# Kernel optimization log

Measured on AMD Instinct MI355X. Metric: run time of the kernel, lower is better.

The kernel has to match this reference:

```python
import jax, jax.numpy as jnp
import numpy as np

T, B, L, CTX, H = 512, 512, 16, 64, 128
STATE_DIM, SHOT, PID, DATA = 32, 12, 35, 23


def setup_inputs() -> dict:
    key = jax.random.key(0)
    ks = jax.random.split(key, 64)
    k = iter(ks)
    def rn(shape, s=0.1):
        return (jax.random.normal(next(k), shape) * s).astype(jnp.float32)
    xs = jax.random.normal(next(k), (T, B, DATA), jnp.float32)
    xs = xs.at[:, :, 12].set(jax.random.randint(next(k), (T, B), 0, SHOT).astype(jnp.float32))
    xs = xs.at[:, :, 17].set(jax.random.randint(next(k), (T, B), 0, PID).astype(jnp.float32))
    xs = xs.at[:, :, 20].set(jax.random.randint(next(k), (T, B), 0, SHOT).astype(jnp.float32))
    return dict(
        total_xs=jnp.zeros((1,), jnp.float32),
        xs=xs,
        ts=jnp.linspace(0.0, 2.0, T).astype(jnp.float32),
        noise_std=jnp.asarray(0.1, jnp.float32),
        z0_noise=jax.random.normal(next(k), (B, L), jnp.float32),
        bm_noise=jax.random.normal(next(k), (T - 1, B, L), jnp.float32),
        shot_emb=rn((SHOT, 8)), player_emb=rn((PID, 8)),
        gru_wih=rn((3 * H, STATE_DIM)), gru_whh=rn((3 * H, H)),
        gru_bih=rn((3 * H,)), gru_bhh=rn((3 * H,)),
        enc_w=rn((CTX, H)), enc_b=rn((CTX,)),
        qz0_w=rn((2 * L, CTX)), qz0_b=rn((2 * L,)),
        f_w1=rn((H, L + CTX)), f_b1=rn((H,)), f_w2=rn((H, H)), f_b2=rn((H,)),
        f_w3=rn((L, H)), f_b3=rn((L,)),
        h_w1=rn((H, L)), h_b1=rn((H,)), h_w2=rn((H, H)), h_b2=rn((H,)),
        h_w3=rn((L, H)), h_b3=rn((L,)),
        g_w1=rn((L, H)), g_b1=rn((L, H)), g_w2=rn((L, H)), g_b2=rn((L,)),
        proj_w=rn((STATE_DIM, L)), proj_b=rn((STATE_DIM,)),
        pz0_mean=jnp.zeros((1, L), jnp.float32), pz0_logstd=jnp.zeros((1, L), jnp.float32),
        act_w=rn((128, L)), act_b=rn((128,)),
        act_land_w=rn((2, 128)), act_shot_w=rn((SHOT, 128)), act_move_w=rn((2, 128)),
    )


def _forward(xs, noise_std, shot_emb, player_emb, gru_wih, gru_whh, gru_bih, gru_bhh,
             enc_w, enc_b, qz0_w, qz0_b,
             f_w1, f_b1, f_w2, f_b2, f_w3, f_b3,
             h_w1, h_b1, h_w2, h_b2, h_w3, h_b3,
             g_w1, g_b1, g_w2, g_b2,
             proj_w, proj_b, pz0_mean, pz0_logstd,
             act_w, act_b, act_land_w, act_shot_w, act_move_w,
             ts, z0_noise, bm_noise):
    # --- SDE_embed_and_transform: replace shot/player id cols with embeddings ---
    state = xs[:, :, :18]
    shot_ids = state[:, :, 12].astype(jnp.int32)
    pid_ids = state[:, :, 17].astype(jnp.int32)
    state_t = jnp.concatenate([state[:, :, :12], shot_emb[shot_ids],
                               state[:, :, 13:17], player_emb[pid_ids]], axis=-1)  # (T,B,32)
    xs_t = jnp.concatenate([state_t, xs[:, :, 18:]], axis=-1)  # (T,B,37)
    # --- Encoder: GRU over time-reversed states, linear head, flip back ---
    def gru_step(h, xt):
        gi = xt @ gru_wih.T + gru_bih
        gh = h @ gru_whh.T + gru_bhh
        ir, iz, inn = jnp.split(gi, 3, axis=-1)
        hr, hz, hn = jnp.split(gh, 3, axis=-1)
        r = jax.nn.sigmoid(ir + hr)
        zg = jax.nn.sigmoid(iz + hz)
        n = jnp.tanh(inn + r * hn)
        hnew = (1.0 - zg) * n + zg * h
        return hnew, hnew
    h0 = jnp.zeros((xs.shape[1], gru_whh.shape[1]), xs.dtype)
    _, hs = jax.lax.scan(gru_step, h0, state_t[::-1])
    ctx = (hs @ enc_w.T + enc_b)[::-1]  # (T,B,CTX)
    # --- posterior z0 ---
    qm, qls = jnp.split(ctx[0] @ qz0_w.T + qz0_b, 2, axis=1)
    z0 = qm + jnp.exp(qls) * z0_noise
    # --- Euler-Maruyama with logqp; searchsorted(right) -> ctx[min(i+1,T-1)] = ctx[i+1] ---
    dts = ts[1:] - ts[:-1]  # (T-1,)
    dW = jnp.sqrt(dts)[:, None, None] * bm_noise
    ctx_steps = ctx[1:]
    def mlp3(x, w1, b1, w2, b2, w3, b3):
        h1 = jax.nn.softplus(x @ w1.T + b1)
        h2 = jax.nn.softplus(h1 @ w2.T + b2)
        return h2 @ w3.T + b3
    def g_diag(y):  # (B,L): per-latent-dim scalar nets, batched over L
        hg = jax.nn.softplus(y[:, :, None] * g_w1[None] + g_b1[None])  # (B,L,H)
        return jax.nn.sigmoid(jnp.einsum('blh,lh->bl', hg, g_w2) + g_b2)
    def sde_step(z, inp):
        c, dw, dt = inp
        f_val = mlp3(jnp.concatenate([z, c], axis=1), f_w1, f_b1, f_w2, f_b2, f_w3, f_b3)
        h_val = mlp3(z, h_w1, h_b1, h_w2, h_b2, h_w3, h_b3)
        g_val = g_diag(z)
        u = (f_val - h_val) / g_val
        logr = 0.5 * jnp.sum(u * u, axis=1) * dt
        z_new = z + f_val * dt + g_val * dw
        return z_new, (z_new, logr)
    _, (z_tail, log_ratio) = jax.lax.scan(sde_step, z0, (ctx_steps, dW, dts))
    zs = jnp.concatenate([z0[None], z_tail], axis=0)  # (T,B,L)
    _xs = zs @ proj_w.T + proj_b  # (T,B,32)
    # --- action model losses ---
    a = jax.nn.relu(zs @ act_w.T + act_b)
    land = (a @ act_land_w.T).reshape(-1, 2)
    shot_logits = (a @ act_shot_w.T).reshape(-1, act_shot_w.shape[0])
    move = (a @ act_move_w.T).reshape(-1, 2)
    true_actions = xs_t[:, :, -5:]
    true_land = true_actions[:, :, :2].reshape(-1, 2)
    true_move = true_actions[:, :, 3:].reshape(-1, 2)
    true_shot = true_actions[:, :, 2].astype(jnp.int32).reshape(-1)
    land_loss = jnp.mean((land - true_land) ** 2)
    move_loss = jnp.mean((move - true_move) ** 2)
    logp = jax.nn.log_softmax(shot_logits, axis=-1)
    picked = jnp.take_along_axis(logp, true_shot[:, None], axis=1)[:, 0]
    mask = (true_shot != 0).astype(logp.dtype)  # CrossEntropy ignore_index=0
    shot_loss = -jnp.sum(picked * mask) / jnp.maximum(jnp.sum(mask), 1.0)
    # --- reconstruction log-likelihood ---
    xs_state = xs_t[:, :, :STATE_DIM]
    LOG2PI = 1.8378770664093453
    log_pxs = jnp.mean(jnp.sum(
        -0.5 * ((xs_state - _xs) / noise_std) ** 2 - jnp.log(noise_std) - 0.5 * LOG2PI,
        axis=(0, 2)))
    # --- KL(q(z0) || p(z0)) ---
    var_q = jnp.exp(2.0 * qls)
    var_p = jnp.exp(2.0 * pz0_logstd)
    kl = pz0_logstd - qls + (var_q + (qm - pz0_mean) ** 2) / (2.0 * var_p) - 0.5
    logqp0 = jnp.mean(jnp.sum(kl, axis=1))
    logqp_path = jnp.mean(jnp.sum(log_ratio, axis=0))
    return log_pxs, logqp0 + logqp_path + land_loss + shot_loss + move_loss


def reference(total_xs, xs, ts, noise_std, z0_noise, bm_noise, shot_emb, player_emb,
              gru_wih, gru_whh, gru_bih, gru_bhh, enc_w, enc_b, qz0_w, qz0_b,
              f_w1, f_b1, f_w2, f_b2, f_w3, f_b3, h_w1, h_b1, h_w2, h_b2, h_w3, h_b3,
              g_w1, g_b1, g_w2, g_b2, proj_w, proj_b, pz0_mean, pz0_logstd,
              act_w, act_b, act_land_w, act_shot_w, act_move_w):
    return _forward(xs, noise_std, shot_emb, player_emb, gru_wih, gru_whh, gru_bih, gru_bhh,
                    enc_w, enc_b, qz0_w, qz0_b,
                    f_w1, f_b1, f_w2, f_b2, f_w3, f_b3,
                    h_w1, h_b1, h_w2, h_b2, h_w3, h_b3,
                    g_w1, g_b1, g_w2, g_b2,
                    proj_w, proj_b, pz0_mean, pz0_logstd,
                    act_w, act_b, act_land_w, act_shot_w, act_move_w,
                    ts, z0_noise, bm_noise)
```

## Files before the change

kernel.cpp:

```cpp
#include <hip/hip_runtime.h>
#include <cstdint>

typedef _Float16 f16;
typedef _Float16 f16x2 __attribute__((ext_vector_type(2)));

#define T_STEPS 512
#define B_SZ 512
#define LOG2PI 1.8378770664093453f

__device__ __forceinline__ uint32_t packh2(float a, float b) {
  f16x2 v; v[0] = (f16)a; v[1] = (f16)b;
  return __builtin_bit_cast(uint32_t, v);
}

__device__ __forceinline__ float fdot2(uint32_t a, uint32_t b, float c) {
#if defined(__AMDGCN__) && __has_builtin(__builtin_amdgcn_fdot2)
  return __builtin_amdgcn_fdot2(__builtin_bit_cast(f16x2, a),
                                __builtin_bit_cast(f16x2, b), c, false);
#else
  f16x2 x = __builtin_bit_cast(f16x2, a), y = __builtin_bit_cast(f16x2, b);
  return c + (float)x[0] * (float)y[0] + (float)x[1] * (float)y[1];
#endif
}

#define DOT4(acc, w0, w1, w2, w3, v)                                     \
  do {                                                                   \
    acc = fdot2((w0), (v).x, acc); acc = fdot2((w1), (v).y, acc);        \
    acc = fdot2((w2), (v).z, acc); acc = fdot2((w3), (v).w, acc);        \
  } while (0)

__device__ __forceinline__ float sigmoidf_(float x) {
  return 1.0f / (1.0f + __expf(-x));
}
__device__ __forceinline__ float tanhf_(float x) {
  float ax = fabsf(x);
  float t = __expf(-2.0f * ax);
  float r = (1.0f - t) / (1.0f + t);
  return copysignf(r, x);
}
__device__ __forceinline__ float softplusf_(float x) {
  return fmaxf(x, 0.0f) + __logf(1.0f + __expf(-fabsf(x)));
}

__global__ __launch_bounds__(256) void k_embed(
    const float* __restrict__ xs, const float* __restrict__ shot_emb,
    const float* __restrict__ player_emb, f16* __restrict__ state_t,
    float* __restrict__ accums) {
  if (blockIdx.x == 0 && threadIdx.x < 16) accums[threadIdx.x] = 0.0f;
  size_t idx = (size_t)blockIdx.x * 256 + threadIdx.x;
  const float* xp = xs + idx * 23;
  f16* op = state_t + idx * 32;
  int sid = (int)xp[12];
  int pid = (int)xp[17];
#pragma unroll
  for (int i = 0; i < 12; ++i) op[i] = (f16)xp[i];
  const float* se = shot_emb + sid * 8;
#pragma unroll
  for (int i = 0; i < 8; ++i) op[12 + i] = (f16)se[i];
#pragma unroll
  for (int i = 0; i < 4; ++i) op[20 + i] = (f16)xp[13 + i];
  const float* pe = player_emb + pid * 8;
#pragma unroll
  for (int i = 0; i < 8; ++i) op[24 + i] = (f16)pe[i];
}

__global__ __launch_bounds__(512) void k_gru(
    const f16* __restrict__ state_t, const float* __restrict__ wih,
    const float* __restrict__ whh, const float* __restrict__ bih,
    const float* __restrict__ bhh, const float* __restrict__ enc_w,
    const float* __restrict__ enc_b, const float* __restrict__ qz0_w,
    const float* __restrict__ qz0_b, const float* __restrict__ z0_noise,
    const float* __restrict__ pz0_mean, const float* __restrict__ pz0_logstd,
    f16* __restrict__ ctx, float* __restrict__ z0_out,
    float* __restrict__ accums) {
  __shared__ uint32_t s_x[2][16];
  __shared__ uint32_t s_h[2][64];
  __shared__ float s_gates[2 * 128 * 4];
  __shared__ float s_encp[2 * 64 * 2];
  __shared__ float s_ctx0[2][64];
  __shared__ float s_q[2][32];

  const int tid = threadIdx.x;
  const int bbase = blockIdx.x * 2;
  const uint32_t* stu = (const uint32_t*)state_t;

  uint32_t wA[64];
  uint32_t wB[16];
  float bias0 = 0.f, bias1 = 0.f, encbr = 0.f;

  if (tid < 256) {
    int g = tid >> 7, du = tid & 127;
    const float* whr = whh + (size_t)(g * 128 + du) * 128;
#pragma unroll
    for (int i = 0; i < 64; ++i) wA[i] = packh2(whr[2 * i], whr[2 * i + 1]);
    const float* wxr = wih + (size_t)(g * 128 + du) * 32;
#pragma unroll
    for (int i = 0; i < 16; ++i) wB[i] = packh2(wxr[2 * i], wxr[2 * i + 1]);
    bias0 = bih[g * 128 + du] + bhh[g * 128 + du];
  } else if (tid < 384) {
    int du = tid - 256;
    const float* whr = whh + (size_t)(256 + du) * 128;
#pragma unroll
    for (int i = 0; i < 64; ++i) wA[i] = packh2(whr[2 * i], whr[2 * i + 1]);
    const float* wxr = wih + (size_t)(256 + du) * 32;
#pragma unroll
    for (int i = 0; i < 16; ++i) wB[i] = packh2(wxr[2 * i], wxr[2 * i + 1]);
    bias0 = bih[256 + du];
    bias1 = bhh[256 + du];
  } else {
    int e = tid - 384, c = e & 63, ks = e >> 6;
    const float* wer = enc_w + (size_t)c * 128 + ks * 64;
#pragma unroll
    for (int i = 0; i < 32; ++i) wA[i] = packh2(wer[2 * i], wer[2 * i + 1]);
    encbr = enc_b[c];
  }

  if (tid < 128) s_h[tid >> 6][tid & 63] = 0u;
  if (tid < 32) {
    int b = tid >> 4, i = tid & 15;
    s_x[b][i] = stu[((size_t)(T_STEPS - 1) * B_SZ + bbase + b) * 16 + i];
  }
  float h_old = 0.0f;
  __syncthreads();

  for (int t = T_STEPS - 1; t >= 0; --t) {
    uint4 xpref = make_uint4(0, 0, 0, 0);
    if (tid < 256) {
      int g = tid >> 7, du = tid & 127;
#pragma unroll
      for (int b = 0; b < 2; ++b) {
        float a = bias0;
        const uint4* xq = (const uint4*)&s_x[b][0];
#pragma unroll
        for (int j = 0; j < 4; ++j) {
          uint4 v = xq[j];
          DOT4(a, wB[4 * j], wB[4 * j + 1], wB[4 * j + 2], wB[4 * j + 3], v);
        }
        const uint4* hq = (const uint4*)&s_h[b][0];
#pragma unroll
        for (int j = 0; j < 16; ++j) {
          uint4 v = hq[j];
          DOT4(a, wA[4 * j], wA[4 * j + 1], wA[4 * j + 2], wA[4 * j + 3], v);
        }
        s_gates[(b * 128 + du) * 4 + g] = a;
      }
    } else if (tid < 384) {
      int du = tid - 256;
#pragma unroll
      for (int b = 0; b < 2; ++b) {
        float aI = bias0, aH = bias1;
        const uint4* xq = (const uint4*)&s_x[b][0];
#pragma unroll
        for (int j = 0; j < 4; ++j) {
          uint4 v = xq[j];
          DOT4(aI, wB[4 * j], wB[4 * j + 1], wB[4 * j + 2], wB[4 * j + 3], v);
        }
        const uint4* hq = (const uint4*)&s_h[b][0];
#pragma unroll
        for (int j = 0; j < 16; ++j) {
          uint4 v = hq[j];
          DOT4(aH, wA[4 * j], wA[4 * j + 1], wA[4 * j + 2], wA[4 * j + 3], v);
        }
        s_gates[(b * 128 + du) * 4 + 2] = aI;
        s_gates[(b * 128 + du) * 4 + 3] = aH;
      }
    } else {
      int e = tid - 384, ks = e >> 6, cc = e & 63;
      (void)cc;
      if (t < T_STEPS - 1) {
#pragma unroll
        for (int b = 0; b < 2; ++b) {
          float a = 0.f;
          const uint4* hq = (const uint4*)&s_h[b][ks * 32];
#pragma unroll
          for (int j = 0; j < 8; ++j) {
            uint4 v = hq[j];
            DOT4(a, wA[4 * j], wA[4 * j + 1], wA[4 * j + 2], wA[4 * j + 3], v);
          }
          s_encp[(b * 64 + cc) * 2 + ks] = a;
        }
      }
      if (e < 8 && t > 0) {
        int b = e & 1, q = e >> 1;
        xpref = *(const uint4*)(stu +
                                ((size_t)(t - 1) * B_SZ + bbase + b) * 16 + q * 4);
      }
    }
    __syncthreads();
    if (tid < 256) {
      int b = tid >> 7, du = tid & 127;
      const float4 gt = *(const float4*)&s_gates[(b * 128 + du) * 4];
      float r = sigmoidf_(gt.x), zg = sigmoidf_(gt.y);
      float n = tanhf_(gt.z + r * gt.w);
      float hnew = (1.0f - zg) * n + zg * h_old;
      h_old = hnew;
      ((f16*)&s_h[b][0])[du] = (f16)hnew;
    } else if (tid >= 384) {
      int e = tid - 384, cc = e & 63, b = e >> 6;
      if (t < T_STEPS - 1) {
        float2 p = *(const float2*)&s_encp[(b * 64 + cc) * 2];
        ctx[((size_t)(t + 1) * B_SZ + bbase + b) * 64 + cc] =
            (f16)(p.x + p.y + encbr);
      }
      if (e < 8 && t > 0) {
        int b2 = e & 1, q = e >> 1;
        *(uint4*)&s_x[b2][q * 4] = xpref;
      }
    }
    __syncthreads();
  }

  if (tid >= 384) {
    int e = tid - 384, ks = e >> 6, cc = e & 63;
#pragma unroll
    for (int b = 0; b < 2; ++b) {
      float a = 0.f;
      const uint4* hq = (const uint4*)&s_h[b][ks * 32];
#pragma unroll
      for (int j = 0; j < 8; ++j) {
        uint4 v = hq[j];
        DOT4(a, wA[4 * j], wA[4 * j + 1], wA[4 * j + 2], wA[4 * j + 3], v);
      }
      s_encp[(b * 64 + cc) * 2 + ks] = a;
    }
  }
  __syncthreads();
  if (tid >= 384) {
    int e = tid - 384, cc = e & 63, b = e >> 6;
    float2 p = *(const float2*)&s_encp[(b * 64 + cc) * 2];
    float val = p.x + p.y + encbr;
    ctx[((size_t)bbase + b) * 64 + cc] = (f16)val;
    s_ctx0[b][cc] = val;
  }
  __syncthreads();
  if (tid < 64) {
    int b = tid >> 5, o = tid & 31;
    float acc = qz0_b[o];
#pragma unroll 8
    for (int k = 0; k < 64; ++k) acc += qz0_w[o * 64 + k] * s_ctx0[b][k];
    s_q[b][o] = acc;
  }
  __syncthreads();
  if (tid < 32) {
    int b = tid >> 4, l = tid & 15;
    int bg = bbase + b;
    float qm = s_q[b][l], qls = s_q[b][16 + l];
    float z0v = qm + __expf(qls) * z0_noise[bg * 16 + l];
    z0_out[bg * 16 + l] = z0v;
    float pm = pz0_mean[l], pls = pz0_logstd[l];
    float var_q = __expf(2.0f * qls);
    float var_p = __expf(2.0f * pls);
    float dm = qm - pm;
    float kl = pls - qls + (var_q + dm * dm) / (2.0f * var_p) - 0.5f;
    atomicAdd(&accums[5], kl);
  }
}

__global__ __launch_bounds__(512) void k_sde(
    const f16* __restrict__ ctx, const float* __restrict__ z0_in,
    const float* __restrict__ ts, const float* __restrict__ bm_noise,
    const float* __restrict__ fw1, const float* __restrict__ fb1,
    const float* __restrict__ fw2, const float* __restrict__ fb2,
    const float* __restrict__ fw3, const float* __restrict__ fb3,
    const float* __restrict__ hw1, const float* __restrict__ hb1,
    const float* __restrict__ hw2, const float* __restrict__ hb2,
    const float* __restrict__ hw3, const float* __restrict__ hb3,
    const float* __restrict__ gw1, const float* __restrict__ gb1,
    const float* __restrict__ gw2, const float* __restrict__ gb2,
    f16* __restrict__ zs, float* __restrict__ accums) {
  __shared__ uint32_t s_x2[2][40];
  __shared__ float s_zf[2][16];
  __shared__ uint32_t s_h1[2][2][64];
  __shared__ uint32_t s_h2[2][2][64];
  __shared__ float s_gp[256];
  __shared__ float s_gv[32];
  __shared__ float s_p2[2 * 2 * 128 * 2];
  __shared__ float s_p3[2 * 2 * 16 * 8];
  __shared__ float s_dts[512];

  const int tid = threadIdx.x;
  const int bbase = blockIdx.x * 2;

  uint32_t uw[48];
  uint32_t wP2[32];
  uint32_t wP3[8];
  float bias1r = 0.f, bias2r = 0.f, gb2r = 0.f, fb3r = 0.f, hb3r = 0.f;

  if (tid < 256) {
    int l = tid & 15, k8 = (tid >> 4) & 7;
#pragma unroll
    for (int i = 0; i < 16; ++i) {
      int h = k8 * 16 + i;
      uw[i] = __builtin_bit_cast(uint32_t, gw1[l * 128 + h]);
      uw[16 + i] = __builtin_bit_cast(uint32_t, gb1[l * 128 + h]);
      uw[32 + i] = __builtin_bit_cast(uint32_t, gw2[l * 128 + h]);
    }
  } else if (tid < 384) {
    int u = tid - 256;
    const float* w = fw1 + (size_t)u * 80;
#pragma unroll
    for (int i = 0; i < 40; ++i) uw[i] = packh2(w[2 * i], w[2 * i + 1]);
    bias1r = fb1[u];
  } else {
    int u = tid - 384;
    const float* w = hw1 + (size_t)u * 16;
#pragma unroll
    for (int i = 0; i < 8; ++i) uw[i] = packh2(w[2 * i], w[2 * i + 1]);
    bias1r = hb1[u];
  }
  {
    int u = tid & 127, ks = (tid >> 7) & 1, mlp = tid >> 8;
    const float* w = (mlp ? hw2 : fw2) + (size_t)u * 128 + ks * 64;
#pragma unroll
    for (int i = 0; i < 32; ++i) wP2[i] = packh2(w[2 * i], w[2 * i + 1]);
    bias2r = (mlp ? hb2 : fb2)[u];
  }
  if (tid < 128 || (tid >= 256 && tid < 384)) {
    int o = tid & 15, k8 = (tid >> 4) & 7;
    const float* w = ((tid >= 256) ? hw3 : fw3) + (size_t)o * 128 + k8 * 16;
#pragma unroll
    for (int i = 0; i < 8; ++i) wP3[i] = packh2(w[2 * i], w[2 * i + 1]);
  }
  if (tid >= 128 && tid < 160) gb2r = gb2[tid & 15];
  if (tid < 32) {
    fb3r = fb3[tid & 15];
    hb3r = hb3[tid & 15];
  }

  if (tid < 511) s_dts[tid] = ts[tid + 1] - ts[tid];
  float bmc = 0.f;
  uint4 cpref = make_uint4(0, 0, 0, 0);
  if (tid < 32) {
    int b = tid >> 4, l = tid & 15, bg = bbase + b;
    float z = z0_in[bg * 16 + l];
    s_zf[b][l] = z;
    ((f16*)&s_x2[b][0])[l] = (f16)z;
    zs[(size_t)bg * 16 + l] = (f16)z;
    bmc = bm_noise[((size_t)0 * B_SZ + bg) * 16 + l];
  }
  if (tid >= 32 && tid < 48) {
    int i = tid - 32, b = i & 1, q = i >> 1;
    const uint32_t* cu = (const uint32_t*)ctx;
    uint4 v = *(const uint4*)(cu + ((size_t)1 * B_SZ + bbase + b) * 32 + q * 4);
    *(uint4*)&s_x2[b][8 + q * 4] = v;
  }
  float path_acc = 0.0f;
  __syncthreads();

  for (int t = 0; t < T_STEPS - 1; ++t) {
    float bmn = 0.f;
    if (tid < 32 && t < T_STEPS - 2) {
      int b = tid >> 4, l = tid & 15, bg = bbase + b;
      bmn = bm_noise[((size_t)(t + 1) * B_SZ + bg) * 16 + l];
    }
    if (tid >= 32 && tid < 48 && t <= T_STEPS - 3) {
      int i = tid - 32, b = i & 1, q = i >> 1;
      const uint32_t* cu = (const uint32_t*)ctx;
      cpref = *(const uint4*)(cu +
                              ((size_t)(t + 2) * B_SZ + bbase + b) * 32 + q * 4);
    }
    if (tid < 256) {
      int b = tid >> 7, l = tid & 15, k8 = (tid >> 4) & 7;
      float y = s_zf[b][l];
      float acc = 0.f;
#pragma unroll
      for (int i = 0; i < 16; ++i) {
        float pre = fmaf(y, __builtin_bit_cast(float, uw[i]),
                         __builtin_bit_cast(float, uw[16 + i]));
        acc = fmaf(softplusf_(pre), __builtin_bit_cast(float, uw[32 + i]), acc);
      }
      s_gp[(b * 16 + l) * 8 + k8] = acc;
    } else if (tid < 384) {
      int u = tid - 256;
#pragma unroll
      for (int b = 0; b < 2; ++b) {
        float a = bias1r;
        const uint4* xq = (const uint4*)&s_x2[b][0];
#pragma unroll
        for (int j = 0; j < 10; ++j) {
          uint4 v = xq[j];
          DOT4(a, uw[4 * j], uw[4 * j + 1], uw[4 * j + 2], uw[4 * j + 3], v);
        }
        ((f16*)&s_h1[0][b][0])[u] = (f16)softplusf_(a);
      }
    } else {
      int u = tid - 384;
#pragma unroll
      for (int b = 0; b < 2; ++b) {
        float a = bias1r;
        const uint4* xq = (const uint4*)&s_x2[b][0];
#pragma unroll
        for (int j = 0; j < 2; ++j) {
          uint4 v = xq[j];
          DOT4(a, uw[4 * j], uw[4 * j + 1], uw[4 * j + 2], uw[4 * j + 3], v);
        }
        ((f16*)&s_h1[1][b][0])[u] = (f16)softplusf_(a);
      }
    }
    __syncthreads();
    {
      int u = tid & 127, ks = (tid >> 7) & 1, mlp = tid >> 8;
#pragma unroll
      for (int b = 0; b < 2; ++b) {
        float a = 0.f;
        const uint4* hq = (const uint4*)&s_h1[mlp][b][ks * 32];
#pragma unroll
        for (int j = 0; j < 8; ++j) {
          uint4 v = hq[j];
          DOT4(a, wP2[4 * j], wP2[4 * j + 1], wP2[4 * j + 2], wP2[4 * j + 3], v);
        }
        s_p2[((mlp * 2 + b) * 128 + u) * 2 + ks] = a;
      }
    }
    __syncthreads();
    {
      int u = tid & 127, b = (tid >> 7) & 1, mlp = tid >> 8;
      float2 p = *(const float2*)&s_p2[((mlp * 2 + b) * 128 + u) * 2];
      ((f16*)&s_h2[mlp][b][0])[u] = (f16)softplusf_(p.x + p.y + bias2r);
    }
    __syncthreads();
    if (tid < 128 || (tid >= 256 && tid < 384)) {
      int o = tid & 15, k8 = (tid >> 4) & 7, mlp = tid >> 8;
#pragma unroll
      for (int b = 0; b < 2; ++b) {
        float a = 0.f;
        const uint4* hq = (const uint4*)&s_h2[mlp][b][k8 * 8];
#pragma unroll
        for (int j = 0; j < 2; ++j) {
          uint4 v = hq[j];
          DOT4(a, wP3[4 * j], wP3[4 * j + 1], wP3[4 * j + 2], wP3[4 * j + 3], v);
        }
        s_p3[((mlp * 2 + b) * 16 + o) * 8 + k8] = a;
      }
    } else if (tid >= 128 && tid < 160) {
      int i = tid - 128, b = i >> 4, l = i & 15;
      const float4* gp = (const float4*)&s_gp[(b * 16 + l) * 8];
      float4 g0 = gp[0], g1 = gp[1];
      float sum = g0.x + g0.y + g0.z + g0.w + g1.x + g1.y + g1.z + g1.w + gb2r;
      s_gv[b * 16 + l] = sigmoidf_(sum);
    }
    __syncthreads();
    if (tid < 32) {
      int b = tid >> 4, l = tid & 15, bg = bbase + b;
      const float4* fp = (const float4*)&s_p3[((0 * 2 + b) * 16 + l) * 8];
      const float4* hp = (const float4*)&s_p3[((2 + b) * 16 + l) * 8];
      float4 f0 = fp[0], f1v = fp[1], h0 = hp[0], h1v = hp[1];
      float fv = fb3r + f0.x + f0.y + f0.z + f0.w + f1v.x + f1v.y + f1v.z + f1v.w;
      float hv = hb3r + h0.x + h0.y + h0.z + h0.w + h1v.x + h1v.y + h1v.z + h1v.w;
      float gv = s_gv[b * 16 + l];
      float dt = s_dts[t];
      float u = (fv - hv) / gv;
      float lsum = u * u;
      lsum += __shfl_xor(lsum, 1);
      lsum += __shfl_xor(lsum, 2);
      lsum += __shfl_xor(lsum, 4);
      lsum += __shfl_xor(lsum, 8);
      if (l == 0) path_acc += 0.5f * lsum * dt;
      float dw = sqrtf(dt) * bmc;
      float zn = s_zf[b][l] + fv * dt + gv * dw;
      s_zf[b][l] = zn;
      ((f16*)&s_x2[b][0])[l] = (f16)zn;
      zs[((size_t)(t + 1) * B_SZ + bg) * 16 + l] = (f16)zn;
      bmc = bmn;
    } else if (tid >= 32 && tid < 48 && t <= T_STEPS - 3) {
      int i = tid - 32, b = i & 1, q = i >> 1;
      *(uint4*)&s_x2[b][8 + q * 4] = cpref;
    }
    __syncthreads();
  }
  if (tid < 32 && (tid & 15) == 0) atomicAdd(&accums[6], path_acc);
}

__global__ __launch_bounds__(256) void k_dec(
    const f16* __restrict__ zs, const f16* __restrict__ state_t,
    const float* __restrict__ xs, const float* __restrict__ proj_w,
    const float* __restrict__ proj_b, const float* __restrict__ act_w,
    const float* __restrict__ act_b, const float* __restrict__ land_w,
    const float* __restrict__ shot_w, const float* __restrict__ move_w,
    float* __restrict__ accums) {
  __shared__ uint32_t s_proj[8 * 32];
  __shared__ uint32_t s_act[8 * 128];
  __shared__ uint32_t s_head[128 * 8];
  __shared__ float s_pb[32], s_ab[128];
  __shared__ float s_red[4 * 5];

  const int tid = threadIdx.x;
  for (int id = tid; id < 8 * 32; id += 256) {
    int kp = id & 7, n = id >> 3;
    s_proj[kp * 32 + n] = packh2(proj_w[n * 16 + 2 * kp], proj_w[n * 16 + 2 * kp + 1]);
  }
  for (int id = tid; id < 8 * 128; id += 256) {
    int kp = id & 7, n = id >> 3;
    s_act[kp * 128 + n] = packh2(act_w[n * 16 + 2 * kp], act_w[n * 16 + 2 * kp + 1]);
  }
  for (int id = tid; id < 128 * 8; id += 256) {
    int j = id >> 3, p = id & 7;
    int h0 = 2 * p, h1 = 2 * p + 1;
    float w0 = (h0 < 2) ? land_w[h0 * 128 + j]
                        : (h0 < 14 ? shot_w[(h0 - 2) * 128 + j]
                                   : move_w[(h0 - 14) * 128 + j]);
    float w1 = (h1 < 2) ? land_w[h1 * 128 + j]
                        : (h1 < 14 ? shot_w[(h1 - 2) * 128 + j]
                                   : move_w[(h1 - 14) * 128 + j]);
    s_head[j * 8 + p] = packh2(w0, w1);
  }
  if (tid < 32) s_pb[tid] = proj_b[tid];
  if (tid < 128) s_ab[tid] = act_b[tid];
  __syncthreads();

  size_t idx = (size_t)blockIdx.x * 256 + tid;
  uint32_t z2[8];
  const uint32_t* zp = (const uint32_t*)(zs + idx * 16);
#pragma unroll
  for (int i = 0; i < 8; ++i) z2[i] = zp[i];
  uint32_t stv[16];
  const uint32_t* stp = (const uint32_t*)(state_t + idx * 32);
#pragma unroll
  for (int i = 0; i < 16; ++i) stv[i] = stp[i];

  float sqsum = 0.0f;
#pragma unroll 4
  for (int i = 0; i < 32; ++i) {
    float acc = s_pb[i];
#pragma unroll
    for (int kp = 0; kp < 8; ++kp) acc = fdot2(s_proj[kp * 32 + i], z2[kp], acc);
    f16x2 sv = __builtin_bit_cast(f16x2, stv[i >> 1]);
    float d = (float)sv[i & 1] - acc;
    sqsum += d * d;
  }

  float hd[16];
#pragma unroll
  for (int i = 0; i < 16; ++i) hd[i] = 0.0f;
#pragma unroll 2
  for (int j = 0; j < 128; ++j) {
    float a = s_ab[j];
#pragma unroll
    for (int kp = 0; kp < 8; ++kp) a = fdot2(s_act[kp * 128 + j], z2[kp], a);
    a = fmaxf(a, 0.0f);
#pragma unroll
    for (int p = 0; p < 8; ++p) {
      f16x2 w = __builtin_bit_cast(f16x2, s_head[j * 8 + p]);
      hd[2 * p] += (float)w[0] * a;
      hd[2 * p + 1] += (float)w[1] * a;
    }
  }
  const float* xp = xs + idx * 23;
  float dl0 = hd[0] - xp[18], dl1 = hd[1] - xp[19];
  float land = dl0 * dl0 + dl1 * dl1;
  float dm0 = hd[14] - xp[21], dm1 = hd[15] - xp[22];
  float move = dm0 * dm0 + dm1 * dm1;
  int sid = (int)xp[20];
  float m = hd[2];
#pragma unroll
  for (int s = 1; s < 12; ++s) m = fmaxf(m, hd[2 + s]);
  float sume = 0.0f;
#pragma unroll
  for (int s = 0; s < 12; ++s) sume += __expf(hd[2 + s] - m);
  float lse = m + __logf(sume);
  float pl = 0.0f;
#pragma unroll
  for (int s = 0; s < 12; ++s)
    if (s == sid) pl = hd[2 + s];
  float picked = 0.0f, cnt = 0.0f;
  if (sid != 0) {
    picked = pl - lse;
    cnt = 1.0f;
  }
  float vals[5] = {sqsum, land, move, picked, cnt};
#pragma unroll
  for (int v = 0; v < 5; ++v) {
    float x = vals[v];
    for (int off = 1; off < 64; off <<= 1) x += __shfl_xor(x, off);
    vals[v] = x;
  }
  int lane = tid & 63, wv = tid >> 6;
  if (lane == 0) {
#pragma unroll
    for (int v = 0; v < 5; ++v) s_red[wv * 5 + v] = vals[v];
  }
  __syncthreads();
  if (tid == 0) {
#pragma unroll
    for (int v = 0; v < 5; ++v) {
      float s = s_red[v] + s_red[5 + v] + s_red[10 + v] + s_red[15 + v];
      atomicAdd(&accums[v], s);
    }
  }
}

__global__ void k_fin(const float* __restrict__ accums,
                      const float* __restrict__ noise_std,
                      float* __restrict__ out) {
  if (threadIdx.x == 0 && blockIdx.x == 0) {
    float sd = noise_std[0];
    float log_pxs = -0.5f * accums[0] / (sd * sd * (float)B_SZ) -
                    (float)T_STEPS * 32.0f * (logf(sd) + 0.5f * LOG2PI);
    float land = accums[1] / (float)(T_STEPS * B_SZ * 2);
    float move = accums[2] / (float)(T_STEPS * B_SZ * 2);
    float shot = -accums[3] / fmaxf(accums[4], 1.0f);
    float out1 = accums[5] / (float)B_SZ + accums[6] / (float)B_SZ + land + shot + move;
    out[0] = log_pxs;
    out[1] = out1;
  }
}

extern "C" void kernel_launch(void* const* d_in, const int* in_sizes, int n_in,
                              void* d_out, int out_size, void* d_ws,
                              size_t ws_size, hipStream_t stream) {
  const float* xs = (const float*)d_in[1];
  const float* ts = (const float*)d_in[2];
  const float* noise_std = (const float*)d_in[3];
  const float* z0_noise = (const float*)d_in[4];
  const float* bm_noise = (const float*)d_in[5];
  const float* shot_emb = (const float*)d_in[6];
  const float* player_emb = (const float*)d_in[7];
  const float* gru_wih = (const float*)d_in[8];
  const float* gru_whh = (const float*)d_in[9];
  const float* gru_bih = (const float*)d_in[10];
  const float* gru_bhh = (const float*)d_in[11];
  const float* enc_w = (const float*)d_in[12];
  const float* enc_b = (const float*)d_in[13];
  const float* qz0_w = (const float*)d_in[14];
  const float* qz0_b = (const float*)d_in[15];
  const float* f_w1 = (const float*)d_in[16];
  const float* f_b1 = (const float*)d_in[17];
  const float* f_w2 = (const float*)d_in[18];
  const float* f_b2 = (const float*)d_in[19];
  const float* f_w3 = (const float*)d_in[20];
  const float* f_b3 = (const float*)d_in[21];
  const float* h_w1 = (const float*)d_in[22];
  const float* h_b1 = (const float*)d_in[23];
  const float* h_w2 = (const float*)d_in[24];
  const float* h_b2 = (const float*)d_in[25];
  const float* h_w3 = (const float*)d_in[26];
  const float* h_b3 = (const float*)d_in[27];
  const float* g_w1 = (const float*)d_in[28];
  const float* g_b1 = (const float*)d_in[29];
  const float* g_w2 = (const float*)d_in[30];
  const float* g_b2 = (const float*)d_in[31];
  const float* proj_w = (const float*)d_in[32];
  const float* proj_b = (const float*)d_in[33];
  const float* pz0_mean = (const float*)d_in[34];
  const float* pz0_logstd = (const float*)d_in[35];
  const float* act_w = (const float*)d_in[36];
  const float* act_b = (const float*)d_in[37];
  const float* act_land_w = (const float*)d_in[38];
  const float* act_shot_w = (const float*)d_in[39];
  const float* act_move_w = (const float*)d_in[40];

  char* ws = (char*)d_ws;
  float* accums = (float*)ws;
  f16* state_t = (f16*)(ws + 256);
  f16* ctx = (f16*)(ws + 256 + 16777216);
  float* z0b = (float*)(ws + 256 + 16777216 + 33554432);
  f16* zs = (f16*)(ws + 256 + 16777216 + 33554432 + 32768);

  k_embed<<<1024, 256, 0, stream>>>(xs, shot_emb, player_emb, state_t, accums);
  k_gru<<<256, 512, 0, stream>>>(state_t, gru_wih, gru_whh, gru_bih, gru_bhh,
                                 enc_w, enc_b, qz0_w, qz0_b, z0_noise, pz0_mean,
                                 pz0_logstd, ctx, z0b, accums);
  k_sde<<<256, 512, 0, stream>>>(ctx, z0b, ts, bm_noise, f_w1, f_b1, f_w2, f_b2,
                                 f_w3, f_b3, h_w1, h_b1, h_w2, h_b2, h_w3, h_b3,
                                 g_w1, g_b1, g_w2, g_b2, zs, accums);
  k_dec<<<1024, 256, 0, stream>>>(zs, state_t, xs, proj_w, proj_b, act_w, act_b,
                                  act_land_w, act_shot_w, act_move_w, accums);
  k_fin<<<1, 64, 0, stream>>>(accums, noise_std, (float*)d_out);
}
```

Measured before the change: 1.996 ms.

## Process one batch element per block in GRU and SDE recurrences

The GRU and SDE recurrent kernels now handle a single batch element per workgroup instead of two, doubling the grid from 256 to 512 blocks. This halves the serial work per timestep inside each block, shortening the latency-bound recurrence chain. Dot products are also split into two independent accumulators to expose more instruction-level parallelism. The cost is that weights are loaded into registers twice as many times, and more blocks must be co-resident (the MI355X has 256 CUs) for the extra blocks to run concurrently rather than in a second wave.

```diff
diff --git a/kernel.cpp b/kernel.cpp
--- a/kernel.cpp
+++ b/kernel.cpp
@@ -73,15 +73,15 @@
     const float* __restrict__ pz0_mean, const float* __restrict__ pz0_logstd,
     f16* __restrict__ ctx, float* __restrict__ z0_out,
     float* __restrict__ accums) {
-  __shared__ uint32_t s_x[2][16];
-  __shared__ uint32_t s_h[2][64];
-  __shared__ float s_gates[2 * 128 * 4];
-  __shared__ float s_encp[2 * 64 * 2];
-  __shared__ float s_ctx0[2][64];
-  __shared__ float s_q[2][32];
+  __shared__ uint32_t s_x[16];
+  __shared__ uint32_t s_h[64];
+  __shared__ float s_gates[128 * 4];
+  __shared__ float s_encp[64 * 2];
+  __shared__ float s_ctx0[64];
+  __shared__ float s_q[32];
 
   const int tid = threadIdx.x;
-  const int bbase = blockIdx.x * 2;
+  const int bg = blockIdx.x;
   const uint32_t* stu = (const uint32_t*)state_t;
 
   uint32_t wA[64];
@@ -115,139 +115,115 @@
     encbr = enc_b[c];
   }
 
-  if (tid < 128) s_h[tid >> 6][tid & 63] = 0u;
-  if (tid < 32) {
-    int b = tid >> 4, i = tid & 15;
-    s_x[b][i] = stu[((size_t)(T_STEPS - 1) * B_SZ + bbase + b) * 16 + i];
-  }
+  if (tid < 64) s_h[tid] = 0u;
+  if (tid < 16) s_x[tid] = stu[((size_t)(T_STEPS - 1) * B_SZ + bg) * 16 + tid];
   float h_old = 0.0f;
   __syncthreads();
 
   for (int t = T_STEPS - 1; t >= 0; --t) {
     uint4 xpref = make_uint4(0, 0, 0, 0);
     if (tid < 256) {
-      int g = tid >> 7, du = tid & 127;
-#pragma unroll
-      for (int b = 0; b < 2; ++b) {
-        float a = bias0;
-        const uint4* xq = (const uint4*)&s_x[b][0];
-#pragma unroll
-        for (int j = 0; j < 4; ++j) {
-          uint4 v = xq[j];
-          DOT4(a, wB[4 * j], wB[4 * j + 1], wB[4 * j + 2], wB[4 * j + 3], v);
-        }
-        const uint4* hq = (const uint4*)&s_h[b][0];
-#pragma unroll
-        for (int j = 0; j < 16; ++j) {
-          uint4 v = hq[j];
-          DOT4(a, wA[4 * j], wA[4 * j + 1], wA[4 * j + 2], wA[4 * j + 3], v);
-        }
-        s_gates[(b * 128 + du) * 4 + g] = a;
-      }
+      float a0 = bias0, a1 = 0.f;
+      const uint4* xq = (const uint4*)&s_x[0];
+#pragma unroll
+      for (int j = 0; j < 4; j += 2) {
+        uint4 v0 = xq[j], v1 = xq[j + 1];
+        DOT4(a0, wB[4 * j], wB[4 * j + 1], wB[4 * j + 2], wB[4 * j + 3], v0);
+        DOT4(a1, wB[4 * j + 4], wB[4 * j + 5], wB[4 * j + 6], wB[4 * j + 7], v1);
+      }
+      const uint4* hq = (const uint4*)&s_h[0];
+#pragma unroll
+      for (int j = 0; j < 16; j += 2) {
+        uint4 v0 = hq[j], v1 = hq[j + 1];
+        DOT4(a0, wA[4 * j], wA[4 * j + 1], wA[4 * j + 2], wA[4 * j + 3], v0);
+        DOT4(a1, wA[4 * j + 4], wA[4 * j + 5], wA[4 * j + 6], wA[4 * j + 7], v1);
+      }
+      s_gates[(tid & 127) * 4 + (tid >> 7)] = a0 + a1;
     } else if (tid < 384) {
-      int du = tid - 256;
-#pragma unroll
-      for (int b = 0; b < 2; ++b) {
-        float aI = bias0, aH = bias1;
-        const uint4* xq = (const uint4*)&s_x[b][0];
-#pragma unroll
-        for (int j = 0; j < 4; ++j) {
-          uint4 v = xq[j];
-          DOT4(aI, wB[4 * j], wB[4 * j + 1], wB[4 * j + 2], wB[4 * j + 3], v);
-        }
-        const uint4* hq = (const uint4*)&s_h[b][0];
-#pragma unroll
-        for (int j = 0; j < 16; ++j) {
-          uint4 v = hq[j];
-          DOT4(aH, wA[4 * j], wA[4 * j + 1], wA[4 * j + 2], wA[4 * j + 3], v);
-        }
-        s_gates[(b * 128 + du) * 4 + 2] = aI;
-        s_gates[(b * 128 + du) * 4 + 3] = aH;
-      }
+      float aI = bias0, aH0 = bias1, aH1 = 0.f;
+      const uint4* xq = (const uint4*)&s_x[0];
+#pragma unroll
+      for (int j = 0; j < 4; ++j) {
+        uint4 v = xq[j];
+        DOT4(aI, wB[4 * j], wB[4 * j + 1], wB[4 * j + 2], wB[4 * j + 3], v);
+      }
+      const uint4* hq = (const uint4*)&s_h[0];
+#pragma unroll
+      for (int j = 0; j < 16; j += 2) {
+        uint4 v0 = hq[j], v1 = hq[j + 1];
+        DOT4(aH0, wA[4 * j], wA[4 * j + 1], wA[4 * j + 2], wA[4 * j + 3], v0);
+        DOT4(aH1, wA[4 * j + 4], wA[4 * j + 5], wA[4 * j + 6], wA[4 * j + 7], v1);
+      }
+      s_gates[(tid - 256) * 4 + 2] = aI;
+      s_gates[(tid - 256) * 4 + 3] = aH0 + aH1;
     } else {
       int e = tid - 384, ks = e >> 6, cc = e & 63;
-      (void)cc;
       if (t < T_STEPS - 1) {
-#pragma unroll
-        for (int b = 0; b < 2; ++b) {
-          float a = 0.f;
-          const uint4* hq = (const uint4*)&s_h[b][ks * 32];
-#pragma unroll
-          for (int j = 0; j < 8; ++j) {
-            uint4 v = hq[j];
-            DOT4(a, wA[4 * j], wA[4 * j + 1], wA[4 * j + 2], wA[4 * j + 3], v);
-          }
-          s_encp[(b * 64 + cc) * 2 + ks] = a;
+        float a0 = 0.f, a1 = 0.f;
+        const uint4* hq = (const uint4*)&s_h[ks * 32];
+#pragma unroll
+        for (int j = 0; j < 8; j += 2) {
+          uint4 v0 = hq[j], v1 = hq[j + 1];
+          DOT4(a0, wA[4 * j], wA[4 * j + 1], wA[4 * j + 2], wA[4 * j + 3], v0);
+          DOT4(a1, wA[4 * j + 4], wA[4 * j + 5], wA[4 * j + 6], wA[4 * j + 7], v1);
         }
-      }
-      if (e < 8 && t > 0) {
-        int b = e & 1, q = e >> 1;
-        xpref = *(const uint4*)(stu +
-                                ((size_t)(t - 1) * B_SZ + bbase + b) * 16 + q * 4);
-      }
+        s_encp[cc * 2 + ks] = a0 + a1;
+      }
+      if (e < 4 && t > 0)
+        xpref = *(const uint4*)(stu + ((size_t)(t - 1) * B_SZ + bg) * 16 + e * 4);
     }
     __syncthreads();
-    if (tid < 256) {
-      int b = tid >> 7, du = tid & 127;
-      const float4 gt = *(const float4*)&s_gates[(b * 128 + du) * 4];
+    if (tid < 128) {
+      const float4 gt = *(const float4*)&s_gates[tid * 4];
       float r = sigmoidf_(gt.x), zg = sigmoidf_(gt.y);
       float n = tanhf_(gt.z + r * gt.w);
       float hnew = (1.0f - zg) * n + zg * h_old;
       h_old = hnew;
-      ((f16*)&s_h[b][0])[du] = (f16)hnew;
+      ((f16*)&s_h[0])[tid] = (f16)hnew;
     } else if (tid >= 384) {
-      int e = tid - 384, cc = e & 63, b = e >> 6;
-      if (t < T_STEPS - 1) {
-        float2 p = *(const float2*)&s_encp[(b * 64 + cc) * 2];
-        ctx[((size_t)(t + 1) * B_SZ + bbase + b) * 64 + cc] =
-            (f16)(p.x + p.y + encbr);
-      }
-      if (e < 8 && t > 0) {
-        int b2 = e & 1, q = e >> 1;
-        *(uint4*)&s_x[b2][q * 4] = xpref;
-      }
+      int e = tid - 384;
+      if (e < 64 && t < T_STEPS - 1) {
+        float2 p = *(const float2*)&s_encp[e * 2];
+        ctx[((size_t)(t + 1) * B_SZ + bg) * 64 + e] = (f16)(p.x + p.y + encbr);
+      }
+      if (e < 4 && t > 0) *(uint4*)&s_x[e * 4] = xpref;
     }
     __syncthreads();
   }
 
   if (tid >= 384) {
     int e = tid - 384, ks = e >> 6, cc = e & 63;
-#pragma unroll
-    for (int b = 0; b < 2; ++b) {
-      float a = 0.f;
-      const uint4* hq = (const uint4*)&s_h[b][ks * 32];
-#pragma unroll
-      for (int j = 0; j < 8; ++j) {
-        uint4 v = hq[j];
-        DOT4(a, wA[4 * j], wA[4 * j + 1], wA[4 * j + 2], wA[4 * j + 3], v);
-      }
-      s_encp[(b * 64 + cc) * 2 + ks] = a;
-    }
+    float a0 = 0.f, a1 = 0.f;
+    const uint4* hq = (const uint4*)&s_h[ks * 32];
+#pragma unroll
+    for (int j = 0; j < 8; j += 2) {
+      uint4 v0 = hq[j], v1 = hq[j + 1];
+      DOT4(a0, wA[4 * j], wA[4 * j + 1], wA[4 * j + 2], wA[4 * j + 3], v0);
+      DOT4(a1, wA[4 * j + 4], wA[4 * j + 5], wA[4 * j + 6], wA[4 * j + 7], v1);
+    }
+    s_encp[cc * 2 + ks] = a0 + a1;
   }
   __syncthreads();
-  if (tid >= 384) {
-    int e = tid - 384, cc = e & 63, b = e >> 6;
-    float2 p = *(const float2*)&s_encp[(b * 64 + cc) * 2];
+  if (tid >= 384 && tid < 448) {
+    int cc = tid - 384;
+    float2 p = *(const float2*)&s_encp[cc * 2];
     float val = p.x + p.y + encbr;
-    ctx[((size_t)bbase + b) * 64 + cc] = (f16)val;
-    s_ctx0[b][cc] = val;
-  }
-  __syncthreads();
-  if (tid < 64) {
-    int b = tid >> 5, o = tid & 31;
-    float acc = qz0_b[o];
-#pragma unroll 8
-    for (int k = 0; k < 64; ++k) acc += qz0_w[o * 64 + k] * s_ctx0[b][k];
-    s_q[b][o] = acc;
+    ctx[(size_t)bg * 64 + cc] = (f16)val;
+    s_ctx0[cc] = val;
   }
   __syncthreads();
   if (tid < 32) {
-    int b = tid >> 4, l = tid & 15;
-    int bg = bbase + b;
-    float qm = s_q[b][l], qls = s_q[b][16 + l];
-    float z0v = qm + __expf(qls) * z0_noise[bg * 16 + l];
-    z0_out[bg * 16 + l] = z0v;
-    float pm = pz0_mean[l], pls = pz0_logstd[l];
+    float acc = qz0_b[tid];
+#pragma unroll 8
+    for (int k = 0; k < 64; ++k) acc += qz0_w[tid * 64 + k] * s_ctx0[k];
+    s_q[tid] = acc;
+  }
+  __syncthreads();
+  if (tid < 16) {
+    float qm = s_q[tid], qls = s_q[16 + tid];
+    float z0v = qm + __expf(qls) * z0_noise[bg * 16 + tid];
+    z0_out[bg * 16 + tid] = z0v;
+    float pm = pz0_mean[tid], pls = pz0_logstd[tid];
     float var_q = __expf(2.0f * qls);
     float var_p = __expf(2.0f * pls);
     float dm = qm - pm;
@@ -268,26 +244,26 @@
     const float* __restrict__ gw1, const float* __restrict__ gb1,
     const float* __restrict__ gw2, const float* __restrict__ gb2,
     f16* __restrict__ zs, float* __restrict__ accums) {
-  __shared__ uint32_t s_x2[2][40];
-  __shared__ float s_zf[2][16];
-  __shared__ uint32_t s_h1[2][2][64];
-  __shared__ uint32_t s_h2[2][2][64];
-  __shared__ float s_gp[256];
-  __shared__ float s_gv[32];
-  __shared__ float s_p2[2 * 2 * 128 * 2];
-  __shared__ float s_p3[2 * 2 * 16 * 8];
+  __shared__ uint32_t s_x2[40];
+  __shared__ float s_zf[16];
+  __shared__ uint32_t s_h1[2][64];
+  __shared__ uint32_t s_h2[2][64];
+  __shared__ float s_gp[128];
+  __shared__ float s_gv[16];
+  __shared__ float s_p2[2 * 128 * 2];
+  __shared__ float s_p3[2 * 16 * 8];
   __shared__ float s_dts[512];
 
   const int tid = threadIdx.x;
-  const int bbase = blockIdx.x * 2;
+  const int bg = blockIdx.x;
 
   uint32_t uw[48];
   uint32_t wP2[32];
   uint32_t wP3[8];
   float bias1r = 0.f, bias2r = 0.f, gb2r = 0.f, fb3r = 0.f, hb3r = 0.f;
 
-  if (tid < 256) {
-    int l = tid & 15, k8 = (tid >> 4) & 7;
+  if (tid < 128) {
+    int l = tid & 15, k8 = tid >> 4;
 #pragma unroll
     for (int i = 0; i < 16; ++i) {
       int h = k8 * 16 + i;
@@ -295,13 +271,13 @@
       uw[16 + i] = __builtin_bit_cast(uint32_t, gb1[l * 128 + h]);
       uw[32 + i] = __builtin_bit_cast(uint32_t, gw2[l * 128 + h]);
     }
-  } else if (tid < 384) {
+  } else if (tid >= 256 && tid < 384) {
     int u = tid - 256;
     const float* w = fw1 + (size_t)u * 80;
 #pragma unroll
     for (int i = 0; i < 40; ++i) uw[i] = packh2(w[2 * i], w[2 * i + 1]);
     bias1r = fb1[u];
-  } else {
+  } else if (tid >= 384) {
     int u = tid - 384;
     const float* w = hw1 + (size_t)u * 16;
 #pragma unroll
@@ -321,47 +297,43 @@
 #pragma unroll
     for (int i = 0; i < 8; ++i) wP3[i] = packh2(w[2 * i], w[2 * i + 1]);
   }
-  if (tid >= 128 && tid < 160) gb2r = gb2[tid & 15];
-  if (tid < 32) {
-    fb3r = fb3[tid & 15];
-    hb3r = hb3[tid & 15];
+  if (tid >= 128 && tid < 144) gb2r = gb2[tid - 128];
+  if (tid < 16) {
+    fb3r = fb3[tid];
+    hb3r = hb3[tid];
   }
 
   if (tid < 511) s_dts[tid] = ts[tid + 1] - ts[tid];
   float bmc = 0.f;
   uint4 cpref = make_uint4(0, 0, 0, 0);
-  if (tid < 32) {
-    int b = tid >> 4, l = tid & 15, bg = bbase + b;
-    float z = z0_in[bg * 16 + l];
-    s_zf[b][l] = z;
-    ((f16*)&s_x2[b][0])[l] = (f16)z;
-    zs[(size_t)bg * 16 + l] = (f16)z;
-    bmc = bm_noise[((size_t)0 * B_SZ + bg) * 16 + l];
-  }
-  if (tid >= 32 && tid < 48) {
-    int i = tid - 32, b = i & 1, q = i >> 1;
+  if (tid < 16) {
+    float z = z0_in[bg * 16 + tid];
+    s_zf[tid] = z;
+    ((f16*)&s_x2[0])[tid] = (f16)z;
+    zs[(size_t)bg * 16 + tid] = (f16)z;
+    bmc = bm_noise[((size_t)0 * B_SZ + bg) * 16 + tid];
+  }
+  if (tid >= 128 && tid < 136) {
+    int q = tid - 128;
     const uint32_t* cu = (const uint32_t*)ctx;
-    uint4 v = *(const uint4*)(cu + ((size_t)1 * B_SZ + bbase + b) * 32 + q * 4);
-    *(uint4*)&s_x2[b][8 + q * 4] = v;
+    uint4 v = *(const uint4*)(cu + ((size_t)1 * B_SZ + bg) * 32 + q * 4);
+    *(uint4*)&s_x2[8 + q * 4] = v;
   }
   float path_acc = 0.0f;
   __syncthreads();
 
   for (int t = 0; t < T_STEPS - 1; ++t) {
     float bmn = 0.f;
-    if (tid < 32 && t < T_STEPS - 2) {
-      int b = tid >> 4, l = tid & 15, bg = bbase + b;
-      bmn = bm_noise[((size_t)(t + 1) * B_SZ + bg) * 16 + l];
-    }
-    if (tid >= 32 && tid < 48 && t <= T_STEPS - 3) {
-      int i = tid - 32, b = i & 1, q = i >> 1;
+    if (tid < 16 && t < T_STEPS - 2)
+      bmn = bm_noise[((size_t)(t + 1) * B_SZ + bg) * 16 + tid];
+    if (tid >= 128 && tid < 136 && t <= T_STEPS - 3) {
+      int q = tid - 128;
       const uint32_t* cu = (const uint32_t*)ctx;
-      cpref = *(const uint4*)(cu +
-                              ((size_t)(t + 2) * B_SZ + bbase + b) * 32 + q * 4);
-    }
-    if (tid < 256) {
-      int b = tid >> 7, l = tid & 15, k8 = (tid >> 4) & 7;
-      float y = s_zf[b][l];
+      cpref = *(const uint4*)(cu + ((size_t)(t + 2) * B_SZ + bg) * 32 + q * 4);
+    }
+    if (tid < 128) {
+      int l = tid & 15;
+      float y = s_zf[l];
       float acc = 0.f;
 #pragma unroll
       for (int i = 0; i < 16; ++i) {
@@ -369,85 +341,75 @@
                          __builtin_bit_cast(float, uw[16 + i]));
         acc = fmaf(softplusf_(pre), __builtin_bit_cast(float, uw[32 + i]), acc);
       }
-      s_gp[(b * 16 + l) * 8 + k8] = acc;
-    } else if (tid < 384) {
+      s_gp[l * 8 + (tid >> 4)] = acc;
+    } else if (tid >= 256 && tid < 384) {
       int u = tid - 256;
-#pragma unroll
-      for (int b = 0; b < 2; ++b) {
-        float a = bias1r;
-        const uint4* xq = (const uint4*)&s_x2[b][0];
-#pragma unroll
-        for (int j = 0; j < 10; ++j) {
-          uint4 v = xq[j];
-          DOT4(a, uw[4 * j], uw[4 * j + 1], uw[4 * j + 2], uw[4 * j + 3], v);
-        }
-        ((f16*)&s_h1[0][b][0])[u] = (f16)softplusf_(a);
-      }
-    } else {
+      float a0 = bias1r, a1 = 0.f;
+      const uint4* xq = (const uint4*)&s_x2[0];
+#pragma unroll
+      for (int j = 0; j < 10; j += 2) {
+        uint4 v0 = xq[j], v1 = xq[j + 1];
+        DOT4(a0, uw[4 * j], uw[4 * j + 1], uw[4 * j + 2], uw[4 * j + 3], v0);
+        DOT4(a1, uw[4 * j + 4], uw[4 * j + 5], uw[4 * j + 6], uw[4 * j + 7], v1);
+      }
+      ((f16*)&s_h1[0][0])[u] = (f16)softplusf_(a0 + a1);
+    } else if (tid >= 384) {
       int u = tid - 384;
-#pragma unroll
-      for (int b = 0; b < 2; ++b) {
-        float a = bias1r;
-        const uint4* xq = (const uint4*)&s_x2[b][0];
-#pragma unroll
-        for (int j = 0; j < 2; ++j) {
-          uint4 v = xq[j];
-          DOT4(a, uw[4 * j], uw[4 * j + 1], uw[4 * j + 2], uw[4 * j + 3], v);
-        }
-        ((f16*)&s_h1[1][b][0])[u] = (f16)softplusf_(a);
-      }
+      float a = bias1r;
+      const uint4* xq = (const uint4*)&s_x2[0];
+#pragma unroll
+      for (int j = 0; j < 2; ++j) {
+        uint4 v = xq[j];
+        DOT4(a, uw[4 * j], uw[4 * j + 1], uw[4 * j + 2], uw[4 * j + 3], v);
+      }
+      ((f16*)&s_h1[1][0])[u] = (f16)softplusf_(a);
     }
     __syncthreads();
     {
       int u = tid & 127, ks = (tid >> 7) & 1, mlp = tid >> 8;
-#pragma unroll
-      for (int b = 0; b < 2; ++b) {
-        float a = 0.f;
-        const uint4* hq = (const uint4*)&s_h1[mlp][b][ks * 32];
-#pragma unroll
-        for (int j = 0; j < 8; ++j) {
-          uint4 v = hq[j];
-          DOT4(a, wP2[4 * j], wP2[4 * j + 1], wP2[4 * j + 2], wP2[4 * j + 3], v);
-        }
-        s_p2[((mlp * 2 + b) * 128 + u) * 2 + ks] = a;
-      }
+      float a0 = 0.f, a1 = 0.f;
+      const uint4* hq = (const uint4*)&s_h1[mlp][ks * 32];
+#pragma unroll
+      for (int j = 0; j < 8; j += 2) {
+        uint4 v0 = hq[j], v1 = hq[j + 1];
+        DOT4(a0, wP2[4 * j], wP2[4 * j + 1], wP2[4 * j + 2], wP2[4 * j + 3], v0);
+        DOT4(a1, wP2[4 * j + 4], wP2[4 * j + 5], wP2[4 * j + 6], wP2[4 * j + 7], v1);
+      }
+      s_p2[(mlp * 128 + u) * 2 + ks] = a0 + a1;
     }
     __syncthreads();
-    {
-      int u = tid & 127, b = (tid >> 7) & 1, mlp = tid >> 8;
-      float2 p = *(const float2*)&s_p2[((mlp * 2 + b) * 128 + u) * 2];
-      ((f16*)&s_h2[mlp][b][0])[u] = (f16)softplusf_(p.x + p.y + bias2r);
+    if (((tid >> 7) & 1) == 0) {
+      int u = tid & 127, mlp = tid >> 8;
+      float2 p = *(const float2*)&s_p2[(mlp * 128 + u) * 2];
+      ((f16*)&s_h2[mlp][0])[u] = (f16)softplusf_(p.x + p.y + bias2r);
     }
     __syncthreads();
     if (tid < 128 || (tid >= 256 && tid < 384)) {
       int o = tid & 15, k8 = (tid >> 4) & 7, mlp = tid >> 8;
-#pragma unroll
-      for (int b = 0; b < 2; ++b) {
-        float a = 0.f;
-        const uint4* hq = (const uint4*)&s_h2[mlp][b][k8 * 8];
-#pragma unroll
-        for (int j = 0; j < 2; ++j) {
-          uint4 v = hq[j];
-          DOT4(a, wP3[4 * j], wP3[4 * j + 1], wP3[4 * j + 2], wP3[4 * j + 3], v);
-        }
-        s_p3[((mlp * 2 + b) * 16 + o) * 8 + k8] = a;
-      }
-    } else if (tid >= 128 && tid < 160) {
-      int i = tid - 128, b = i >> 4, l = i & 15;
-      const float4* gp = (const float4*)&s_gp[(b * 16 + l) * 8];
+      float a = 0.f;
+      const uint4* hq = (const uint4*)&s_h2[mlp][k8 * 8];
+#pragma unroll
+      for (int j = 0; j < 2; ++j) {
+        uint4 v = hq[j];
+        DOT4(a, wP3[4 * j], wP3[4 * j + 1], wP3[4 * j + 2], wP3[4 * j + 3], v);
+      }
+      s_p3[(mlp * 16 + o) * 8 + k8] = a;
+    } else if (tid >= 128 && tid < 144) {
+      int l = tid - 128;
+      const float4* gp = (const float4*)&s_gp[l * 8];
       float4 g0 = gp[0], g1 = gp[1];
       float sum = g0.x + g0.y + g0.z + g0.w + g1.x + g1.y + g1.z + g1.w + gb2r;
-      s_gv[b * 16 + l] = sigmoidf_(sum);
+      s_gv[l] = sigmoidf_(sum);
     }
     __syncthreads();
-    if (tid < 32) {
-      int b = tid >> 4, l = tid & 15, bg = bbase + b;
-      const float4* fp = (const float4*)&s_p3[((0 * 2 + b) * 16 + l) * 8];
-      const float4* hp = (const float4*)&s_p3[((2 + b) * 16 + l) * 8];
+    if (tid < 16) {
+      int l = tid;
+      const float4* fp = (const float4*)&s_p3[(0 * 16 + l) * 8];
+      const float4* hp = (const float4*)&s_p3[(16 + l) * 8];
       float4 f0 = fp[0], f1v = fp[1], h0 = hp[0], h1v = hp[1];
       float fv = fb3r + f0.x + f0.y + f0.z + f0.w + f1v.x + f1v.y + f1v.z + f1v.w;
       float hv = hb3r + h0.x + h0.y + h0.z + h0.w + h1v.x + h1v.y + h1v.z + h1v.w;
-      float gv = s_gv[b * 16 + l];
+      float gv = s_gv[l];
       float dt = s_dts[t];
       float u = (fv - hv) / gv;
       float lsum = u * u;
@@ -457,18 +419,18 @@
       lsum += __shfl_xor(lsum, 8);
       if (l == 0) path_acc += 0.5f * lsum * dt;
       float dw = sqrtf(dt) * bmc;
-      float zn = s_zf[b][l] + fv * dt + gv * dw;
-      s_zf[b][l] = zn;
-      ((f16*)&s_x2[b][0])[l] = (f16)zn;
+      float zn = s_zf[l] + fv * dt + gv * dw;
+      s_zf[l] = zn;
+      ((f16*)&s_x2[0])[l] = (f16)zn;
       zs[((size_t)(t + 1) * B_SZ + bg) * 16 + l] = (f16)zn;
       bmc = bmn;
-    } else if (tid >= 32 && tid < 48 && t <= T_STEPS - 3) {
-      int i = tid - 32, b = i & 1, q = i >> 1;
-      *(uint4*)&s_x2[b][8 + q * 4] = cpref;
+    } else if (tid >= 128 && tid < 136 && t <= T_STEPS - 3) {
+      int q = tid - 128;
+      *(uint4*)&s_x2[8 + q * 4] = cpref;
     }
     __syncthreads();
   }
-  if (tid < 32 && (tid & 15) == 0) atomicAdd(&accums[6], path_acc);
+  if (tid == 0) atomicAdd(&accums[6], path_acc);
 }
 
 __global__ __launch_bounds__(256) void k_dec(
@@ -657,10 +619,10 @@
   f16* zs = (f16*)(ws + 256 + 16777216 + 33554432 + 32768);
 
   k_embed<<<1024, 256, 0, stream>>>(xs, shot_emb, player_emb, state_t, accums);
-  k_gru<<<256, 512, 0, stream>>>(state_t, gru_wih, gru_whh, gru_bih, gru_bhh,
+  k_gru<<<512, 512, 0, stream>>>(state_t, gru_wih, gru_whh, gru_bih, gru_bhh,
                                  enc_w, enc_b, qz0_w, qz0_b, z0_noise, pz0_mean,
                                  pz0_logstd, ctx, z0b, accums);
-  k_sde<<<256, 512, 0, stream>>>(ctx, z0b, ts, bm_noise, f_w1, f_b1, f_w2, f_b2,
+  k_sde<<<512, 512, 0, stream>>>(ctx, z0b, ts, bm_noise, f_w1, f_b1, f_w2, f_b2,
                                  f_w3, f_b3, h_w1, h_b1, h_w2, h_b2, h_w3, h_b3,
                                  g_w1, g_b1, g_w2, g_b2, zs, accums);
   k_dec<<<1024, 256, 0, stream>>>(zs, state_t, xs, proj_w, proj_b, act_w, act_b,
```

Result: slower. 2.879 ms (+44.3%).
